# Performance work log

Hardware: AMD Instinct MI355X
Metric: run time of the kernel (lower is better)

## Reference

```python
import jax, jax.numpy as jnp
import numpy as np

NEG_SLOPE = 0.01


def reference(feat_src, feat_dst, src, dst, attn_l, attn_r):
    # feat_src: [Ns, D], feat_dst: [Nd, D], src/dst: [E] int, attn_*: [1, D]
    n_dst = feat_dst.shape[0]
    el = (feat_src * attn_l).sum(axis=-1)  # [Ns]
    er = (feat_dst * attn_r).sum(axis=-1)  # [Nd]
    e = el[src] + er[dst]                  # [E]
    e = jnp.where(e >= 0, e, NEG_SLOPE * e)  # leaky_relu
    # edge softmax over incoming edges of each destination node
    m = jax.ops.segment_max(e, dst, num_segments=n_dst)  # [Nd]
    m = jnp.where(jnp.isfinite(m), m, 0.0)  # guard empty segments
    a = jnp.exp(e - m[dst])                 # [E]
    denom = jax.ops.segment_sum(a, dst, num_segments=n_dst)  # [Nd]
    denom = jnp.where(denom > 0, denom, 1.0)
    a = a / denom[dst]
    # weighted scatter-sum of source features: [E, D] messages -> [Nd, D]
    msg = feat_src[src] * a[:, None]
    out = jax.ops.segment_sum(msg, dst, num_segments=n_dst)
    return out


def setup_inputs() -> dict:
    key = jax.random.key(0)
    k1, k2, k3, k4, k5, k6 = jax.random.split(key, 6)
    Ns, Nd, E, D = 100000, 100000, 1600000, 128
    return {
        "feat_src": jax.random.normal(k1, (Ns, D), dtype=jnp.float32),
        "feat_dst": jax.random.normal(k2, (Nd, D), dtype=jnp.float32),
        "src": jax.random.randint(k3, (E,), 0, Ns, dtype=jnp.int32),
        "dst": jax.random.randint(k4, (E,), 0, Nd, dtype=jnp.int32),
        "attn_l": jax.random.normal(k5, (1, D), dtype=jnp.float32) * 0.1,
        "attn_r": jax.random.normal(k6, (1, D), dtype=jnp.float32) * 0.1,
    }
```

## Files before the change

kernel.cpp:

```cpp
#include <hip/hip_runtime.h>
#include <hip/hip_bf16.h>
#include <math.h>

#define D 128
#define AGG_THREADS 128
#define CHUNK 512
#define BSHIFT 8
#define MAXB 1024
#define MAXWG 1024
#define PCHUNK 4096
#define PE 16
#define EBUF_CAP 5120
#define PR 8192

__device__ __forceinline__ unsigned short f2bf(float f) {
    union { float f; unsigned int u; } c; c.f = f;
    unsigned int u = c.u;
    unsigned int r = (u + 0x7FFFu + ((u >> 16) & 1u)) >> 16;
    return (unsigned short)r;
}
__device__ __forceinline__ void unpack2(unsigned int w, float& lo, float& hi) {
    union { unsigned int u; float f; } c;
    c.u = w << 16;          lo = c.f;
    c.u = w & 0xFFFF0000u;  hi = c.f;
}

__global__ void prep_kernel(const float* __restrict__ feat_src,
                            const float* __restrict__ feat_dst,
                            const float* __restrict__ attn_l,
                            const float* __restrict__ attn_r,
                            float* __restrict__ el, float* __restrict__ er,
                            unsigned short* __restrict__ feat_bf, int store_bf,
                            int Ns, int Nd) {
    int half = threadIdx.x >> 5;
    int lane = threadIdx.x & 31;
    int node = blockIdx.x * 8 + half;
    if (node >= Ns + Nd) return;
    bool is_src = node < Ns;
    const float* feat = is_src ? feat_src + (size_t)node * D
                               : feat_dst + (size_t)(node - Ns) * D;
    const float* attn = is_src ? attn_l : attn_r;
    float4 a = ((const float4*)attn)[lane];
    float4 v = ((const float4*)feat)[lane];
    if (is_src && store_bf) {
        ushort4 h; h.x = f2bf(v.x); h.y = f2bf(v.y); h.z = f2bf(v.z); h.w = f2bf(v.w);
        ((ushort4*)(feat_bf + (size_t)node * D))[lane] = h;
    }
    float s = v.x * a.x + v.y * a.y + v.z * a.z + v.w * a.w;
    #pragma unroll
    for (int off = 16; off > 0; off >>= 1)
        s += __shfl_xor(s, off, 64);
    if (lane == 0) {
        if (is_src) el[node] = s;
        else        er[node - Ns] = s;
    }
}

__global__ void partition_kernel(const int* __restrict__ src, const int* __restrict__ dst,
                                 int E, int nbk,
                                 uint2* __restrict__ bins,
                                 int* __restrict__ cnt_tab, int* __restrict__ loc_tab) {
    __shared__ int hist[MAXB];
    __shared__ int lstart[MAXB];
    __shared__ int cursor[MAXB];
    __shared__ uint2 sbuf[PCHUNK];
    int w = blockIdx.x, tid = threadIdx.x;
    int e0 = w * PCHUNK;
    int e1 = min(E, e0 + PCHUNK);
    int n = e1 - e0;

    for (int i = tid; i < nbk; i += 256) hist[i] = 0;
    __syncthreads();

    int es[PE], ed[PE];
    #pragma unroll
    for (int k = 0; k < PE; ++k) {
        int idx = e0 + k * 256 + tid;
        if (idx < e1) {
            es[k] = src[idx];
            ed[k] = dst[idx];
            atomicAdd(&hist[ed[k] >> BSHIFT], 1);
        }
    }
    __syncthreads();

    if (tid < 64) {
        int carry = 0;
        for (int c = 0; c < nbk; c += 64) {
            int i = c + tid;
            int v = (i < nbk) ? hist[i] : 0;
            int x = v;
            #pragma unroll
            for (int off = 1; off < 64; off <<= 1) {
                int t = __shfl_up(x, off, 64);
                if (tid >= off) x += t;
            }
            if (i < nbk) lstart[i] = x - v + carry;
            carry += __shfl(x, 63, 64);
        }
    }
    __syncthreads();

    for (int i = tid; i < nbk; i += 256) {
        cnt_tab[(size_t)w * nbk + i] = hist[i];
        loc_tab[(size_t)w * nbk + i] = lstart[i];
        cursor[i] = 0;
    }
    __syncthreads();

    #pragma unroll
    for (int k = 0; k < PE; ++k) {
        int idx = e0 + k * 256 + tid;
        if (idx < e1) {
            int b = ed[k] >> BSHIFT;
            int r = lstart[b] + atomicAdd(&cursor[b], 1);
            sbuf[r] = make_uint2((unsigned)es[k], (unsigned)ed[k]);
        }
    }
    __syncthreads();

    uint2* obase = bins + (size_t)w * PCHUNK;
    for (int t = tid; t < n; t += 256) obase[t] = sbuf[t];
}

__global__ void bucket_kernel(const uint2* __restrict__ bins,
                              const int* __restrict__ cnt_tab, const int* __restrict__ loc_tab,
                              int nbk, int nwg,
                              int* __restrict__ counts, int* __restrict__ offs,
                              int* __restrict__ perm, int Nd) {
    __shared__ uint2 ebuf[EBUF_CAP];
    __shared__ int wcnt[MAXWG];
    __shared__ int wdst[MAXWG];
    __shared__ int cnt256[256];
    __shared__ int off256[256];
    __shared__ int cur256[256];
    __shared__ int tile[256];
    __shared__ int total_sh;

    int b = blockIdx.x, tid = threadIdx.x;
    int base = b << BSHIFT;

    for (int i = tid; i < nwg; i += 256) wcnt[i] = cnt_tab[(size_t)i * nbk + b];
    __syncthreads();
    if (tid < 64) {
        int carry = 0;
        for (int c = 0; c < nwg; c += 64) {
            int i = c + tid;
            int v = (i < nwg) ? wcnt[i] : 0;
            int x = v;
            #pragma unroll
            for (int off = 1; off < 64; off <<= 1) {
                int t = __shfl_up(x, off, 64);
                if (tid >= off) x += t;
            }
            if (i < nwg) wdst[i] = x - v + carry;
            carry += __shfl(x, 63, 64);
        }
        if (tid == 0) total_sh = carry;
    }
    cnt256[tid] = 0;
    cur256[tid] = 0;
    __syncthreads();
    int n = total_sh;
    bool fits = (n <= EBUF_CAP);

    if (fits) {
        for (int w = tid; w < nwg; w += 256) {
            int c = wcnt[w];
            if (c) {
                const uint2* sp = bins + (size_t)w * PCHUNK + loc_tab[(size_t)w * nbk + b];
                int d0 = wdst[w];
                for (int k = 0; k < c; ++k) ebuf[d0 + k] = sp[k];
            }
        }
        __syncthreads();
        for (int t = tid; t < n; t += 256)
            atomicAdd(&cnt256[(int)ebuf[t].y - base], 1);
    } else {
        for (int w = tid; w < nwg; w += 256) {
            int c = wcnt[w];
            const uint2* sp = bins + (size_t)w * PCHUNK + loc_tab[(size_t)w * nbk + b];
            for (int k = 0; k < c; ++k)
                atomicAdd(&cnt256[(int)sp[k].y - base], 1);
        }
        __syncthreads();
    }
    __syncthreads();

    int v = cnt256[tid];
    tile[tid] = v;
    __syncthreads();
    for (int off = 1; off < 256; off <<= 1) {
        int t = (tid >= off) ? tile[tid - off] : 0;
        __syncthreads();
        tile[tid] += t;
        __syncthreads();
    }
    int myoff = tile[tid] - v;
    off256[tid] = myoff;
    int i = base + tid;
    if (i < Nd) {
        int c = v;
        if (myoff + c > PR) c = max(0, PR - myoff);
        counts[i] = c;
        offs[i]   = myoff;
    }
    __syncthreads();

    size_t rbase = (size_t)b * PR;
    if (fits) {
        for (int t = tid; t < n; t += 256) {
            uint2 e = ebuf[t];
            int d = (int)e.y - base;
            int r = atomicAdd(&cur256[d], 1);
            int slot = off256[d] + r;
            if (slot < PR) perm[rbase + slot] = (int)e.x;
        }
    } else {
        for (int w = tid; w < nwg; w += 256) {
            int c = wcnt[w];
            const uint2* sp = bins + (size_t)w * PCHUNK + loc_tab[(size_t)w * nbk + b];
            for (int k = 0; k < c; ++k) {
                uint2 e = sp[k];
                int d = (int)e.y - base;
                int r = atomicAdd(&cur256[d], 1);
                int slot = off256[d] + r;
                if (slot < PR) perm[rbase + slot] = (int)e.x;
            }
        }
    }
}

__device__ __forceinline__ float block_max128(float v, float* red, int tid) {
    #pragma unroll
    for (int off = 32; off > 0; off >>= 1)
        v = fmaxf(v, __shfl_down(v, off, 64));
    __syncthreads();
    if ((tid & 63) == 0) red[tid >> 6] = v;
    __syncthreads();
    return fmaxf(red[0], red[1]);
}
__device__ __forceinline__ float block_sum128(float v, float* red, int tid) {
    #pragma unroll
    for (int off = 32; off > 0; off >>= 1)
        v += __shfl_down(v, off, 64);
    __syncthreads();
    if ((tid & 63) == 0) red[tid >> 6] = v;
    __syncthreads();
    return red[0] + red[1];
}

__global__ void gat_aggregate_bf16_kernel(const unsigned short* __restrict__ feat_bf,
                                          const float* __restrict__ el,
                                          const float* __restrict__ er,
                                          const int* __restrict__ offs,
                                          const int* __restrict__ counts,
                                          const int* __restrict__ perm,
                                          float* __restrict__ out, int Nd) {
    __shared__ float w_sh[CHUNK];
    __shared__ int   s_sh[CHUNK];
    __shared__ float red[2];
    __shared__ float acc_sh[8][D];

    int j = blockIdx.x;
    int tid = threadIdx.x;
    int cnt = counts[j];
    size_t orow = (size_t)j * D;
    if (cnt == 0) { out[orow + tid] = 0.0f; return; }

    size_t beg = (size_t)(j >> BSHIFT) * PR + offs[j];
    float erj = er[j];
    int g = tid >> 4, u = tid & 15;
    float acc[8];
    #pragma unroll
    for (int k = 0; k < 8; ++k) acc[k] = 0.0f;
    float inv;
    const unsigned short* fb = feat_bf + (size_t)u * 8;

    if (cnt <= CHUNK) {
        float lmax = -INFINITY;
        for (int t = tid; t < cnt; t += AGG_THREADS) {
            int s = perm[beg + t];
            float e = el[s] + erj;
            e = (e >= 0.0f) ? e : 0.01f * e;
            s_sh[t] = s;
            w_sh[t] = e;
            lmax = fmaxf(lmax, e);
        }
        float m = block_max128(lmax, red, tid);
        float lsum = 0.0f;
        for (int t = tid; t < cnt; t += AGG_THREADS) {
            float a = __expf(w_sh[t] - m);
            w_sh[t] = a;
            lsum += a;
        }
        float den = block_sum128(lsum, red, tid);
        inv = 1.0f / den;
        __syncthreads();
        for (int t = g; t < cnt; t += 8) {
            int s = s_sh[t];
            float w = w_sh[t];
            uint4 v = *(const uint4*)(fb + (size_t)s * D);
            float f[8];
            unpack2(v.x, f[0], f[1]); unpack2(v.y, f[2], f[3]);
            unpack2(v.z, f[4], f[5]); unpack2(v.w, f[6], f[7]);
            #pragma unroll
            for (int k = 0; k < 8; ++k) acc[k] += w * f[k];
        }
    } else {
        float lmax = -INFINITY;
        for (int t = tid; t < cnt; t += AGG_THREADS) {
            int s = perm[beg + t];
            float e = el[s] + erj;
            e = (e >= 0.0f) ? e : 0.01f * e;
            lmax = fmaxf(lmax, e);
        }
        float m = block_max128(lmax, red, tid);
        float lsum = 0.0f;
        for (int t = tid; t < cnt; t += AGG_THREADS) {
            int s = perm[beg + t];
            float e = el[s] + erj;
            e = (e >= 0.0f) ? e : 0.01f * e;
            lsum += __expf(e - m);
        }
        float den = block_sum128(lsum, red, tid);
        inv = 1.0f / den;
        for (int bb = 0; bb < cnt; bb += CHUNK) {
            int n = min(CHUNK, cnt - bb);
            __syncthreads();
            for (int t = tid; t < n; t += AGG_THREADS) {
                int s = perm[beg + bb + t];
                float e = el[s] + erj;
                e = (e >= 0.0f) ? e : 0.01f * e;
                s_sh[t] = s;
                w_sh[t] = __expf(e - m);
            }
            __syncthreads();
            for (int t = g; t < n; t += 8) {
                int s = s_sh[t];
                float w = w_sh[t];
                uint4 v = *(const uint4*)(fb + (size_t)s * D);
                float f[8];
                unpack2(v.x, f[0], f[1]); unpack2(v.y, f[2], f[3]);
                unpack2(v.z, f[4], f[5]); unpack2(v.w, f[6], f[7]);
                #pragma unroll
                for (int k = 0; k < 8; ++k) acc[k] += w * f[k];
            }
        }
    }
    #pragma unroll
    for (int k = 0; k < 8; ++k) acc_sh[g][u * 8 + k] = acc[k];
    __syncthreads();
    float r = 0.0f;
    #pragma unroll
    for (int g2 = 0; g2 < 8; ++g2) r += acc_sh[g2][tid];
    out[orow + tid] = r * inv;
}

__global__ void hist_kernel(const int* __restrict__ dst, int E, int* __restrict__ counts) {
    int stride = gridDim.x * blockDim.x;
    for (int k = blockIdx.x * blockDim.x + threadIdx.x; k < E; k += stride)
        atomicAdd(&counts[dst[k]], 1);
}
__global__ void scan1_kernel(const int* __restrict__ counts, int* __restrict__ offsets,
                             int* __restrict__ blockSums, int N) {
    __shared__ int tile[256];
    int tid = threadIdx.x;
    int i = blockIdx.x * 256 + tid;
    int v = (i < N) ? counts[i] : 0;
    tile[tid] = v;
    __syncthreads();
    for (int off = 1; off < 256; off <<= 1) {
        int t = (tid >= off) ? tile[tid - off] : 0;
        __syncthreads();
        tile[tid] += t;
        __syncthreads();
    }
    int incl = tile[tid];
    if (i < N) offsets[i] = incl - v;
    if (tid == 255) blockSums[blockIdx.x] = incl;
}
__global__ void scan2_kernel(int* __restrict__ bs, int nb) {
    __shared__ int tile[256];
    int tid = threadIdx.x;
    int carry = 0;
    for (int base = 0; base < nb; base += 256) {
        int i = base + tid;
        int v = (i < nb) ? bs[i] : 0;
        __syncthreads();
        tile[tid] = v;
        __syncthreads();
        for (int off = 1; off < 256; off <<= 1) {
            int t = (tid >= off) ? tile[tid - off] : 0;
            __syncthreads();
            tile[tid] += t;
            __syncthreads();
        }
        int incl = tile[tid];
        if (i < nb) bs[i] = incl - v + carry;
        carry += tile[255];
    }
}
__global__ void fill_kernel(const int* __restrict__ src, const int* __restrict__ dst, int E,
                            const int* __restrict__ offsets, const int* __restrict__ bsum,
                            int* __restrict__ cursor, int* __restrict__ perm_src) {
    int stride = gridDim.x * blockDim.x;
    for (int k = blockIdx.x * blockDim.x + threadIdx.x; k < E; k += stride) {
        int j = dst[k];
        int p = offsets[j] + bsum[j >> BSHIFT] + atomicAdd(&cursor[j], 1);
        perm_src[p] = src[k];
    }
}
__global__ void gat_aggregate_f32_kernel(const float* __restrict__ feat_src,
                                         const float* __restrict__ el,
                                         const float* __restrict__ er,
                                         const int* __restrict__ offsets,
                                         const int* __restrict__ bsum,
                                         const int* __restrict__ counts,
                                         const int* __restrict__ perm_src,
                                         float* __restrict__ out, int Nd) {
    __shared__ float w_sh[CHUNK];
    __shared__ int   s_sh[CHUNK];
    __shared__ float red[2];
    int j = blockIdx.x;
    int tid = threadIdx.x;
    int cnt = counts[j];
    size_t orow = (size_t)j * D;
    if (cnt == 0) { out[orow + tid] = 0.0f; return; }
    int beg = offsets[j] + bsum[j >> BSHIFT];
    float erj = er[j];
    float acc = 0.0f;
    float inv;
    if (cnt <= CHUNK) {
        float lmax = -INFINITY;
        for (int t = tid; t < cnt; t += AGG_THREADS) {
            int s = perm_src[beg + t];
            float e = el[s] + erj;
            e = (e >= 0.0f) ? e : 0.01f * e;
            s_sh[t] = s; w_sh[t] = e;
            lmax = fmaxf(lmax, e);
        }
        float m = block_max128(lmax, red, tid);
        float lsum = 0.0f;
        for (int t = tid; t < cnt; t += AGG_THREADS) {
            float a = __expf(w_sh[t] - m);
            w_sh[t] = a; lsum += a;
        }
        float den = block_sum128(lsum, red, tid);
        inv = 1.0f / den;
        __syncthreads();
        for (int t = 0; t < cnt; ++t)
            acc += feat_src[(size_t)s_sh[t] * D + tid] * w_sh[t];
    } else {
        float lmax = -INFINITY;
        for (int t = tid; t < cnt; t += AGG_THREADS) {
            int s = perm_src[beg + t];
            float e = el[s] + erj;
            e = (e >= 0.0f) ? e : 0.01f * e;
            lmax = fmaxf(lmax, e);
        }
        float m = block_max128(lmax, red, tid);
        float lsum = 0.0f;
        for (int t = tid; t < cnt; t += AGG_THREADS) {
            int s = perm_src[beg + t];
            float e = el[s] + erj;
            e = (e >= 0.0f) ? e : 0.01f * e;
            lsum += __expf(e - m);
        }
        float den = block_sum128(lsum, red, tid);
        inv = 1.0f / den;
        for (int bb = 0; bb < cnt; bb += CHUNK) {
            int n = min(CHUNK, cnt - bb);
            __syncthreads();
            for (int t = tid; t < n; t += AGG_THREADS) {
                int s = perm_src[beg + bb + t];
                float e = el[s] + erj;
                e = (e >= 0.0f) ? e : 0.01f * e;
                s_sh[t] = s;
                w_sh[t] = __expf(e - m);
            }
            __syncthreads();
            for (int t = 0; t < n; ++t)
                acc += feat_src[(size_t)s_sh[t] * D + tid] * w_sh[t];
        }
    }
    out[orow + tid] = acc * inv;
}

extern "C" void kernel_launch(void* const* d_in, const int* in_sizes, int n_in,
                              void* d_out, int out_size, void* d_ws, size_t ws_size,
                              hipStream_t stream) {
    const float* feat_src = (const float*)d_in[0];
    const float* feat_dst = (const float*)d_in[1];
    const int*   src      = (const int*)d_in[2];
    const int*   dst      = (const int*)d_in[3];
    const float* attn_l   = (const float*)d_in[4];
    const float* attn_r   = (const float*)d_in[5];
    float* out = (float*)d_out;

    int Ns = in_sizes[0] / D;
    int Nd = in_sizes[1] / D;
    int E  = in_sizes[2];
    int NBK = (Nd + (1 << BSHIFT) - 1) >> BSHIFT;
    int NWG = (E + PCHUNK - 1) / PCHUNK;

    char* p = (char*)d_ws;
    auto carve = [&](size_t bytes) { void* r = (void*)p; p += (bytes + 255) & ~(size_t)255; return r; };
    float* el      = (float*)carve((size_t)Ns * 4);
    float* er      = (float*)carve((size_t)Nd * 4);
    int*   counts  = (int*)carve((size_t)Nd * 4);
    int*   offs    = (int*)carve((size_t)Nd * 4);
    int*   gcursor = (int*)carve((size_t)Nd * 4);
    int*   bsums   = (int*)carve((size_t)NBK * 4);
    int*   cnt_tab = (int*)carve((size_t)NWG * NBK * 4);
    int*   loc_tab = (int*)carve((size_t)NWG * NBK * 4);
    int*   perm    = (int*)carve((size_t)NBK * PR * 4);
    uint2* bins    = (uint2*)carve((size_t)NWG * PCHUNK * 8);
    size_t used    = (size_t)(p - (char*)d_ws);
    size_t bf_bytes = (size_t)Ns * D * 2;
    unsigned short* feat_bf = (unsigned short*)carve(bf_bytes);

    int fast = (NBK <= MAXB && NWG <= MAXWG &&
                used + bf_bytes + 256 <= ws_size) ? 1 : 0;

    int total = Ns + Nd;
    if (fast) {
        prep_kernel<<<(total + 7) / 8, 256, 0, stream>>>(feat_src, feat_dst, attn_l, attn_r,
                                                         el, er, feat_bf, 1, Ns, Nd);
        partition_kernel<<<NWG, 256, 0, stream>>>(src, dst, E, NBK, bins, cnt_tab, loc_tab);
        bucket_kernel<<<NBK, 256, 0, stream>>>(bins, cnt_tab, loc_tab, NBK, NWG,
                                               counts, offs, perm, Nd);
        gat_aggregate_bf16_kernel<<<Nd, AGG_THREADS, 0, stream>>>(feat_bf, el, er, offs,
                                                                  counts, perm, out, Nd);
    } else {
        hipMemsetAsync(counts, 0, (size_t)Nd * 4, stream);
        hipMemsetAsync(gcursor, 0, (size_t)Nd * 4, stream);
        prep_kernel<<<(total + 7) / 8, 256, 0, stream>>>(feat_src, feat_dst, attn_l, attn_r,
                                                         el, er, nullptr, 0, Ns, Nd);
        hist_kernel<<<2048, 256, 0, stream>>>(dst, E, counts);
        scan1_kernel<<<NBK, 256, 0, stream>>>(counts, offs, bsums, Nd);
        scan2_kernel<<<1, 256, 0, stream>>>(bsums, NBK);
        fill_kernel<<<2048, 256, 0, stream>>>(src, dst, E, offs, bsums, gcursor, perm);
        gat_aggregate_f32_kernel<<<Nd, AGG_THREADS, 0, stream>>>(feat_src, el, er, offs,
                                                                 bsums, counts, perm, out, Nd);
    }
}
```

Baseline: 276.5 us.

## Merge prep and partition kernels, pack edges into 32 bits, parallelize bucket gather

Combines the feature-prep kernel and the edge-partition kernel into one launch, with the first NWG blocks partitioning edges and the rest computing el/er and the bf16 copy. Edges are packed into one 32-bit word (24-bit source index plus the low 8 bits of dst), which halves bin traffic and shared buffer size. The bucket kernel gathers its edges with a per-element binary search over the per-workgroup prefix offsets, so threads stay busy even when a workgroup contributes a long run. The trade-off is a hard limit of Ns up to 2^24 on the fast path and the extra binary-search work for each element.

```diff
diff --git a/kernel.cpp b/kernel.cpp
--- a/kernel.cpp
+++ b/kernel.cpp
@@ -25,112 +25,116 @@
     c.u = w & 0xFFFF0000u;  hi = c.f;
 }
 
-__global__ void prep_kernel(const float* __restrict__ feat_src,
-                            const float* __restrict__ feat_dst,
-                            const float* __restrict__ attn_l,
-                            const float* __restrict__ attn_r,
-                            float* __restrict__ el, float* __restrict__ er,
-                            unsigned short* __restrict__ feat_bf, int store_bf,
-                            int Ns, int Nd) {
-    int half = threadIdx.x >> 5;
-    int lane = threadIdx.x & 31;
-    int node = blockIdx.x * 8 + half;
-    if (node >= Ns + Nd) return;
-    bool is_src = node < Ns;
-    const float* feat = is_src ? feat_src + (size_t)node * D
-                               : feat_dst + (size_t)(node - Ns) * D;
-    const float* attn = is_src ? attn_l : attn_r;
-    float4 a = ((const float4*)attn)[lane];
-    float4 v = ((const float4*)feat)[lane];
-    if (is_src && store_bf) {
-        ushort4 h; h.x = f2bf(v.x); h.y = f2bf(v.y); h.z = f2bf(v.z); h.w = f2bf(v.w);
-        ((ushort4*)(feat_bf + (size_t)node * D))[lane] = h;
-    }
-    float s = v.x * a.x + v.y * a.y + v.z * a.z + v.w * a.w;
-    #pragma unroll
-    for (int off = 16; off > 0; off >>= 1)
-        s += __shfl_xor(s, off, 64);
-    if (lane == 0) {
-        if (is_src) el[node] = s;
-        else        er[node - Ns] = s;
-    }
-}
-
-__global__ void partition_kernel(const int* __restrict__ src, const int* __restrict__ dst,
-                                 int E, int nbk,
-                                 uint2* __restrict__ bins,
-                                 int* __restrict__ cnt_tab, int* __restrict__ loc_tab) {
+__global__ __launch_bounds__(256) void phase1_kernel(
+        const float* __restrict__ feat_src, const float* __restrict__ feat_dst,
+        const float* __restrict__ attn_l,  const float* __restrict__ attn_r,
+        float* __restrict__ el, float* __restrict__ er,
+        unsigned short* __restrict__ feat_bf,
+        const int* __restrict__ src, const int* __restrict__ dst,
+        int E, int nbk, int nwg,
+        unsigned* __restrict__ bins, int* __restrict__ cnt_tab, int* __restrict__ loc_tab,
+        int Ns, int Nd) {
     __shared__ int hist[MAXB];
     __shared__ int lstart[MAXB];
     __shared__ int cursor[MAXB];
-    __shared__ uint2 sbuf[PCHUNK];
-    int w = blockIdx.x, tid = threadIdx.x;
-    int e0 = w * PCHUNK;
-    int e1 = min(E, e0 + PCHUNK);
-    int n = e1 - e0;
-
-    for (int i = tid; i < nbk; i += 256) hist[i] = 0;
-    __syncthreads();
-
-    int es[PE], ed[PE];
-    #pragma unroll
-    for (int k = 0; k < PE; ++k) {
-        int idx = e0 + k * 256 + tid;
-        if (idx < e1) {
-            es[k] = src[idx];
-            ed[k] = dst[idx];
-            atomicAdd(&hist[ed[k] >> BSHIFT], 1);
-        }
-    }
-    __syncthreads();
-
-    if (tid < 64) {
-        int carry = 0;
-        for (int c = 0; c < nbk; c += 64) {
-            int i = c + tid;
-            int v = (i < nbk) ? hist[i] : 0;
-            int x = v;
-            #pragma unroll
-            for (int off = 1; off < 64; off <<= 1) {
-                int t = __shfl_up(x, off, 64);
-                if (tid >= off) x += t;
-            }
-            if (i < nbk) lstart[i] = x - v + carry;
-            carry += __shfl(x, 63, 64);
-        }
-    }
-    __syncthreads();
-
-    for (int i = tid; i < nbk; i += 256) {
-        cnt_tab[(size_t)w * nbk + i] = hist[i];
-        loc_tab[(size_t)w * nbk + i] = lstart[i];
-        cursor[i] = 0;
-    }
-    __syncthreads();
-
-    #pragma unroll
-    for (int k = 0; k < PE; ++k) {
-        int idx = e0 + k * 256 + tid;
-        if (idx < e1) {
-            int b = ed[k] >> BSHIFT;
-            int r = lstart[b] + atomicAdd(&cursor[b], 1);
-            sbuf[r] = make_uint2((unsigned)es[k], (unsigned)ed[k]);
-        }
-    }
-    __syncthreads();
-
-    uint2* obase = bins + (size_t)w * PCHUNK;
-    for (int t = tid; t < n; t += 256) obase[t] = sbuf[t];
-}
-
-__global__ void bucket_kernel(const uint2* __restrict__ bins,
-                              const int* __restrict__ cnt_tab, const int* __restrict__ loc_tab,
-                              int nbk, int nwg,
-                              int* __restrict__ counts, int* __restrict__ offs,
-                              int* __restrict__ perm, int Nd) {
-    __shared__ uint2 ebuf[EBUF_CAP];
+    __shared__ unsigned sbuf[PCHUNK];
+    int tid = threadIdx.x;
+
+    if ((int)blockIdx.x < nwg) {
+        int w = blockIdx.x;
+        int e0 = w * PCHUNK;
+        int e1 = min(E, e0 + PCHUNK);
+        int n = e1 - e0;
+
+        for (int i = tid; i < nbk; i += 256) hist[i] = 0;
+        __syncthreads();
+
+        unsigned pv[PE]; int bk[PE];
+        #pragma unroll
+        for (int k = 0; k < PE; ++k) {
+            int idx = e0 + k * 256 + tid;
+            if (idx < e1) {
+                int s = src[idx], j = dst[idx];
+                bk[k] = j >> BSHIFT;
+                pv[k] = (unsigned)s | ((unsigned)(j & 255) << 24);
+                atomicAdd(&hist[bk[k]], 1);
+            }
+        }
+        __syncthreads();
+
+        if (tid < 64) {
+            int carry = 0;
+            for (int c = 0; c < nbk; c += 64) {
+                int i = c + tid;
+                int v = (i < nbk) ? hist[i] : 0;
+                int x = v;
+                #pragma unroll
+                for (int off = 1; off < 64; off <<= 1) {
+                    int t = __shfl_up(x, off, 64);
+                    if (tid >= off) x += t;
+                }
+                if (i < nbk) lstart[i] = x - v + carry;
+                carry += __shfl(x, 63, 64);
+            }
+        }
+        __syncthreads();
+
+        for (int i = tid; i < nbk; i += 256) {
+            cnt_tab[(size_t)w * nbk + i] = hist[i];
+            loc_tab[(size_t)w * nbk + i] = lstart[i];
+            cursor[i] = 0;
+        }
+        __syncthreads();
+
+        #pragma unroll
+        for (int k = 0; k < PE; ++k) {
+            int idx = e0 + k * 256 + tid;
+            if (idx < e1) {
+                int b = bk[k];
+                int r = lstart[b] + atomicAdd(&cursor[b], 1);
+                sbuf[r] = pv[k];
+            }
+        }
+        __syncthreads();
+
+        unsigned* obase = bins + (size_t)w * PCHUNK;
+        for (int t = tid; t < n; t += 256) obase[t] = sbuf[t];
+    } else {
+        int blk = blockIdx.x - nwg;
+        int half = tid >> 5, lane = tid & 31;
+        int node = blk * 8 + half;
+        if (node >= Ns + Nd) return;
+        bool is_src = node < Ns;
+        const float* feat = is_src ? feat_src + (size_t)node * D
+                                   : feat_dst + (size_t)(node - Ns) * D;
+        const float* attn = is_src ? attn_l : attn_r;
+        float4 a = ((const float4*)attn)[lane];
+        float4 v = ((const float4*)feat)[lane];
+        if (is_src) {
+            ushort4 h; h.x = f2bf(v.x); h.y = f2bf(v.y); h.z = f2bf(v.z); h.w = f2bf(v.w);
+            ((ushort4*)(feat_bf + (size_t)node * D))[lane] = h;
+        }
+        float s = v.x * a.x + v.y * a.y + v.z * a.z + v.w * a.w;
+        #pragma unroll
+        for (int off = 16; off > 0; off >>= 1)
+            s += __shfl_xor(s, off, 64);
+        if (lane == 0) {
+            if (is_src) el[node] = s;
+            else        er[node - Ns] = s;
+        }
+    }
+}
+
+__global__ __launch_bounds__(256) void bucket_kernel(
+        const unsigned* __restrict__ bins,
+        const int* __restrict__ cnt_tab, const int* __restrict__ loc_tab,
+        int nbk, int nwg,
+        int* __restrict__ counts, int* __restrict__ offs,
+        int* __restrict__ perm, int Nd) {
+    __shared__ unsigned ebuf[EBUF_CAP];
     __shared__ int wcnt[MAXWG];
     __shared__ int wdst[MAXWG];
+    __shared__ int wloc[MAXWG];
     __shared__ int cnt256[256];
     __shared__ int off256[256];
     __shared__ int cur256[256];
@@ -140,7 +144,10 @@
     int b = blockIdx.x, tid = threadIdx.x;
     int base = b << BSHIFT;
 
-    for (int i = tid; i < nwg; i += 256) wcnt[i] = cnt_tab[(size_t)i * nbk + b];
+    for (int i = tid; i < nwg; i += 256) {
+        wcnt[i] = cnt_tab[(size_t)i * nbk + b];
+        wloc[i] = loc_tab[(size_t)i * nbk + b];
+    }
     __syncthreads();
     if (tid < 64) {
         int carry = 0;
@@ -165,25 +172,21 @@
     bool fits = (n <= EBUF_CAP);
 
     if (fits) {
-        for (int w = tid; w < nwg; w += 256) {
-            int c = wcnt[w];
-            if (c) {
-                const uint2* sp = bins + (size_t)w * PCHUNK + loc_tab[(size_t)w * nbk + b];
-                int d0 = wdst[w];
-                for (int k = 0; k < c; ++k) ebuf[d0 + k] = sp[k];
-            }
+        for (int t = tid; t < n; t += 256) {
+            int lo = 0, hi = nwg - 1;
+            while (lo < hi) { int mid = (lo + hi + 1) >> 1; if (wdst[mid] <= t) lo = mid; else hi = mid - 1; }
+            ebuf[t] = bins[(size_t)lo * PCHUNK + wloc[lo] + (t - wdst[lo])];
         }
         __syncthreads();
         for (int t = tid; t < n; t += 256)
-            atomicAdd(&cnt256[(int)ebuf[t].y - base], 1);
+            atomicAdd(&cnt256[ebuf[t] >> 24], 1);
     } else {
         for (int w = tid; w < nwg; w += 256) {
             int c = wcnt[w];
-            const uint2* sp = bins + (size_t)w * PCHUNK + loc_tab[(size_t)w * nbk + b];
+            const unsigned* sp = bins + (size_t)w * PCHUNK + wloc[w];
             for (int k = 0; k < c; ++k)
-                atomicAdd(&cnt256[(int)sp[k].y - base], 1);
-        }
-        __syncthreads();
+                atomicAdd(&cnt256[sp[k] >> 24], 1);
+        }
     }
     __syncthreads();
 
@@ -210,22 +213,22 @@
     size_t rbase = (size_t)b * PR;
     if (fits) {
         for (int t = tid; t < n; t += 256) {
-            uint2 e = ebuf[t];
-            int d = (int)e.y - base;
+            unsigned e = ebuf[t];
+            int d = e >> 24;
             int r = atomicAdd(&cur256[d], 1);
             int slot = off256[d] + r;
-            if (slot < PR) perm[rbase + slot] = (int)e.x;
+            if (slot < PR) perm[rbase + slot] = (int)(e & 0xFFFFFFu);
         }
     } else {
         for (int w = tid; w < nwg; w += 256) {
             int c = wcnt[w];
-            const uint2* sp = bins + (size_t)w * PCHUNK + loc_tab[(size_t)w * nbk + b];
+            const unsigned* sp = bins + (size_t)w * PCHUNK + wloc[w];
             for (int k = 0; k < c; ++k) {
-                uint2 e = sp[k];
-                int d = (int)e.y - base;
+                unsigned e = sp[k];
+                int d = e >> 24;
                 int r = atomicAdd(&cur256[d], 1);
                 int slot = off256[d] + r;
-                if (slot < PR) perm[rbase + slot] = (int)e.x;
+                if (slot < PR) perm[rbase + slot] = (int)(e & 0xFFFFFFu);
             }
         }
     }
@@ -357,6 +360,30 @@
     out[orow + tid] = r * inv;
 }
 
+__global__ void prep_fb_kernel(const float* __restrict__ feat_src,
+                               const float* __restrict__ feat_dst,
+                               const float* __restrict__ attn_l,
+                               const float* __restrict__ attn_r,
+                               float* __restrict__ el, float* __restrict__ er,
+                               int Ns, int Nd) {
+    int half = threadIdx.x >> 5, lane = threadIdx.x & 31;
+    int node = blockIdx.x * 8 + half;
+    if (node >= Ns + Nd) return;
+    bool is_src = node < Ns;
+    const float* feat = is_src ? feat_src + (size_t)node * D
+                               : feat_dst + (size_t)(node - Ns) * D;
+    const float* attn = is_src ? attn_l : attn_r;
+    float4 a = ((const float4*)attn)[lane];
+    float4 v = ((const float4*)feat)[lane];
+    float s = v.x * a.x + v.y * a.y + v.z * a.z + v.w * a.w;
+    #pragma unroll
+    for (int off = 16; off > 0; off >>= 1)
+        s += __shfl_xor(s, off, 64);
+    if (lane == 0) {
+        if (is_src) el[node] = s;
+        else        er[node - Ns] = s;
+    }
+}
 __global__ void hist_kernel(const int* __restrict__ dst, int E, int* __restrict__ counts) {
     int stride = gridDim.x * blockDim.x;
     for (int k = blockIdx.x * blockDim.x + threadIdx.x; k < E; k += stride)
@@ -506,28 +533,29 @@
 
     char* p = (char*)d_ws;
     auto carve = [&](size_t bytes) { void* r = (void*)p; p += (bytes + 255) & ~(size_t)255; return r; };
-    float* el      = (float*)carve((size_t)Ns * 4);
-    float* er      = (float*)carve((size_t)Nd * 4);
-    int*   counts  = (int*)carve((size_t)Nd * 4);
-    int*   offs    = (int*)carve((size_t)Nd * 4);
-    int*   gcursor = (int*)carve((size_t)Nd * 4);
-    int*   bsums   = (int*)carve((size_t)NBK * 4);
-    int*   cnt_tab = (int*)carve((size_t)NWG * NBK * 4);
-    int*   loc_tab = (int*)carve((size_t)NWG * NBK * 4);
-    int*   perm    = (int*)carve((size_t)NBK * PR * 4);
-    uint2* bins    = (uint2*)carve((size_t)NWG * PCHUNK * 8);
-    size_t used    = (size_t)(p - (char*)d_ws);
-    size_t bf_bytes = (size_t)Ns * D * 2;
+    float*    el      = (float*)carve((size_t)Ns * 4);
+    float*    er      = (float*)carve((size_t)Nd * 4);
+    int*      counts  = (int*)carve((size_t)Nd * 4);
+    int*      offs    = (int*)carve((size_t)Nd * 4);
+    int*      gcursor = (int*)carve((size_t)Nd * 4);
+    int*      bsums   = (int*)carve((size_t)NBK * 4);
+    int*      cnt_tab = (int*)carve((size_t)NWG * NBK * 4);
+    int*      loc_tab = (int*)carve((size_t)NWG * NBK * 4);
+    int*      perm    = (int*)carve((size_t)NBK * PR * 4);
+    unsigned* bins    = (unsigned*)carve((size_t)NWG * PCHUNK * 4);
+    size_t used       = (size_t)(p - (char*)d_ws);
+    size_t bf_bytes   = (size_t)Ns * D * 2;
     unsigned short* feat_bf = (unsigned short*)carve(bf_bytes);
 
-    int fast = (NBK <= MAXB && NWG <= MAXWG &&
+    int fast = (NBK <= MAXB && NWG <= MAXWG && Ns <= (1 << 24) &&
                 used + bf_bytes + 256 <= ws_size) ? 1 : 0;
 
     int total = Ns + Nd;
+    int prep_blocks = (total + 7) / 8;
     if (fast) {
-        prep_kernel<<<(total + 7) / 8, 256, 0, stream>>>(feat_src, feat_dst, attn_l, attn_r,
-                                                         el, er, feat_bf, 1, Ns, Nd);
-        partition_kernel<<<NWG, 256, 0, stream>>>(src, dst, E, NBK, bins, cnt_tab, loc_tab);
+        phase1_kernel<<<NWG + prep_blocks, 256, 0, stream>>>(
+            feat_src, feat_dst, attn_l, attn_r, el, er, feat_bf,
+            src, dst, E, NBK, NWG, bins, cnt_tab, loc_tab, Ns, Nd);
         bucket_kernel<<<NBK, 256, 0, stream>>>(bins, cnt_tab, loc_tab, NBK, NWG,
                                                counts, offs, perm, Nd);
         gat_aggregate_bf16_kernel<<<Nd, AGG_THREADS, 0, stream>>>(feat_bf, el, er, offs,
@@ -535,8 +563,8 @@
     } else {
         hipMemsetAsync(counts, 0, (size_t)Nd * 4, stream);
         hipMemsetAsync(gcursor, 0, (size_t)Nd * 4, stream);
-        prep_kernel<<<(total + 7) / 8, 256, 0, stream>>>(feat_src, feat_dst, attn_l, attn_r,
-                                                         el, er, nullptr, 0, Ns, Nd);
+        prep_fb_kernel<<<prep_blocks, 256, 0, stream>>>(feat_src, feat_dst, attn_l, attn_r,
+                                                        el, er, Ns, Nd);
         hist_kernel<<<2048, 256, 0, stream>>>(dst, E, counts);
         scan1_kernel<<<NBK, 256, 0, stream>>>(counts, offs, bsums, Nd);
         scan2_kernel<<<1, 256, 0, stream>>>(bsums, NBK);
```

Measured after the change: 279.7 us. Within noise of the previous version (+1.2%).
